# Kernel optimization log

Measured on AMD Instinct MI355X. Metric: run time of the kernel, lower is better.

## Reference

```python
import jax, jax.numpy as jnp
import numpy as np

NUM_BUCKETS = 320
MAX_DISTANCE = 800


def _layer_norm(x, w, b, eps=1e-5):
    x32 = x.astype(jnp.float32)
    mu = x32.mean(-1, keepdims=True)
    var = x32.var(-1, keepdims=True)
    return ((x32 - mu) / jnp.sqrt(var + eps) * w + b).astype(x.dtype)


def _rel_pos_bucket(rel):
    half = NUM_BUCKETS // 2            # 160
    st = half // 2                     # 80 (small threshold)
    sign = (rel >= 0).astype(jnp.int32)
    ab = jnp.abs(rel)
    is_small = ab < st
    log_ratio = jnp.log(jnp.clip(ab.astype(jnp.float32), 1.0) / st) / np.float32(np.log(MAX_DISTANCE / st))
    log_pos = st + (log_ratio * (half - st)).astype(jnp.int32)  # trunc toward zero like .long()
    log_pos = jnp.minimum(log_pos, half - 1)
    bucket = jnp.where(is_small, ab, log_pos) + sign * half
    return jnp.clip(bucket, 0, NUM_BUCKETS - 1)


def setup_inputs() -> dict:
    key = jax.random.key(0)
    B, T, C, H, FF = 2, 2048, 768, 12, 3072
    D = C // H
    ks = jax.random.split(key, 16)
    s = 0.02
    return {
        "x": jax.random.normal(ks[0], (B, T, C), jnp.float32),
        "ln1_w": jnp.ones((C,), jnp.float32),
        "ln1_b": jnp.zeros((C,), jnp.float32),
        "wq": jax.random.normal(ks[1], (C, C), jnp.float32) * s,
        "bq": jnp.zeros((C,), jnp.float32),
        "wk": jax.random.normal(ks[2], (C, C), jnp.float32) * s,
        "bk": jnp.zeros((C,), jnp.float32),
        "wv": jax.random.normal(ks[3], (C, C), jnp.float32) * s,
        "bv": jnp.zeros((C,), jnp.float32),
        "wo": jax.random.normal(ks[4], (C, C), jnp.float32) * s,
        "bo": jnp.zeros((C,), jnp.float32),
        "ln2_w": jnp.ones((C,), jnp.float32),
        "ln2_b": jnp.zeros((C,), jnp.float32),
        "w1": jax.random.normal(ks[5], (FF, C), jnp.float32) * s,
        "b1": jnp.zeros((FF,), jnp.float32),
        "w2": jax.random.normal(ks[6], (C, FF), jnp.float32) * s,
        "b2": jnp.zeros((C,), jnp.float32),
        "rel_embed": jax.random.normal(ks[7], (NUM_BUCKETS, H), jnp.float32),
        "gate_ur_w": jax.random.normal(ks[8], (H, D), jnp.float32) * 0.01,
        "gate_i_w": jax.random.normal(ks[9], (H, D), jnp.float32) * 0.01,
        "rel_scale": jnp.ones((H,), jnp.float32),
    }


def reference(x, ln1_w, ln1_b, wq, bq, wk, bk, wv, bv, wo, bo,
              ln2_w, ln2_b, w1, b1, w2, b2, rel_embed, gate_ur_w, gate_i_w, rel_scale):
    B, T, C = x.shape
    H = rel_embed.shape[1]
    D = C // H

    residual = x
    h = _layer_norm(x, ln1_w, ln1_b)
    q = (h @ wq.T + bq).reshape(B, T, H, D).transpose(0, 2, 1, 3)  # [B,H,T,D]
    k = (h @ wk.T + bk).reshape(B, T, H, D).transpose(0, 2, 1, 3)
    v = (h @ wv.T + bv).reshape(B, T, H, D).transpose(0, 2, 1, 3)

    attn = jnp.einsum('bhqd,bhkd->bhqk', q, k) * (D ** -0.5)

    # gated relative position bias
    pos = jnp.arange(T)
    rel = pos[None, :] - pos[:, None]                 # [T,T]
    buckets = _rel_pos_bucket(rel)                    # [T,T]
    pe = rel_embed[buckets]                           # [T,T,H]
    pe = jnp.transpose(pe, (2, 0, 1))[None]           # [1,H,T,T]
    g_in = q.mean(axis=2).transpose(0, 2, 1).mean(axis=-1)   # [B,D]
    gate_r = jax.nn.sigmoid(g_in @ gate_ur_w.T)       # [B,H]
    gate_u = jax.nn.sigmoid(g_in @ gate_i_w.T)        # [B,H]
    gate = 1.0 + (gate_u * rel_scale[None, :] * gate_r)[:, :, None, None]
    bias = pe * gate                                  # [B,H,T,T]

    attn = jax.nn.softmax(attn + bias, axis=-1)
    out = jnp.einsum('bhqk,bhkd->bhqd', attn, v).transpose(0, 2, 1, 3).reshape(B, T, C)
    x = residual + out @ wo.T + bo

    residual = x
    h = _layer_norm(x, ln2_w, ln2_b)
    h = jax.nn.gelu(h @ w1.T + b1, approximate=False) @ w2.T + b2
    return residual + h
```

## Files before the change

### kernel.cpp

```cpp
#include <hip/hip_runtime.h>
#include <hip/hip_bf16.h>


#define Tn 2048
#define Cn 768
#define Hn 12
#define Dn 64
#define FFn 3072
#define Mn 4096
#define QKVS 2304
#define LQK 1536

typedef __attribute__((ext_vector_type(8))) short bfrag;
typedef __attribute__((ext_vector_type(8))) unsigned short us8;
typedef __attribute__((ext_vector_type(4))) float f32x4;

#define GLDS(gptr, lptr) __builtin_amdgcn_global_load_lds( \
    (const __attribute__((address_space(1))) void*)(gptr), \
    (__attribute__((address_space(3))) void*)(lptr), 16, 0, 0)

#define SBAR()   __builtin_amdgcn_s_barrier()
#define WAITVM(N) asm volatile("s_waitcnt vmcnt(" #N ")" ::: "memory")
#define WAITLG0() asm volatile("s_waitcnt lgkmcnt(0)" ::: "memory")

#define QSCALE 0.18033688f
#define INVQS  5.5451774445f

__device__ __forceinline__ unsigned short f2bu(float f){
  __hip_bfloat16 h = __float2bfloat16(f);
  return *(unsigned short*)&h;
}
__device__ __forceinline__ float bu2f(unsigned short u){
  union { unsigned int i; float f; } v; v.i = ((unsigned int)u) << 16; return v.f;
}
__device__ __forceinline__ us8 pack8(float4 a, float4 b){
  us8 c;
  c[0]=f2bu(a.x); c[1]=f2bu(a.y); c[2]=f2bu(a.z); c[3]=f2bu(a.w);
  c[4]=f2bu(b.x); c[5]=f2bu(b.y); c[6]=f2bu(b.z); c[7]=f2bu(b.w);
  return c;
}
__device__ __forceinline__ float fexp2(float x){ return __builtin_amdgcn_exp2f(x); }

__device__ __forceinline__ float block_reduce_sum(float v, float* sred){
  #pragma unroll
  for (int off = 32; off > 0; off >>= 1) v += __shfl_down(v, off, 64);
  __syncthreads();
  if ((threadIdx.x & 63) == 0) sred[threadIdx.x >> 6] = v;
  __syncthreads();
  return sred[0] + sred[1] + sred[2] + sred[3];
}

__global__ __launch_bounds__(256) void cast_all_kernel(
    const float* __restrict__ wq, const float* __restrict__ wk,
    const float* __restrict__ wv, const float* __restrict__ wo,
    const float* __restrict__ w1, const float* __restrict__ w2,
    const float* __restrict__ bq, const float* __restrict__ bk,
    const float* __restrict__ bv, const float* __restrict__ rel_embed,
    unsigned short* __restrict__ Wqkv, unsigned short* __restrict__ Wob,
    unsigned short* __restrict__ W1b, unsigned short* __restrict__ W2b,
    float* __restrict__ bias_rel, float* __restrict__ bqkv)
{
  const int blk = blockIdx.x;
  if (blk >= 3472){
    const int i = (blk - 3472) * 256 + threadIdx.x;
    bqkv[i] = (i < Cn) ? bq[i] : (i < 2 * Cn) ? bk[i - Cn] : bv[i - 2 * Cn];
    return;
  }
  if (blk >= 3456){
    const int idx = (blk - 3456) * 256 + threadIdx.x;
    if (idx >= 4095) return;
    const int rel = idx - 2047;
    const int ab = rel < 0 ? -rel : rel;
    int bucket;
    if (ab < 80){
      bucket = ab;
    } else {
      const float lr = logf((float)ab * (1.0f / 80.0f)) * (1.0f / 2.3025851f);
      int lp = 80 + (int)(lr * 80.0f);
      bucket = lp < 159 ? lp : 159;
    }
    if (rel >= 0) bucket += 160;
    #pragma unroll
    for (int h = 0; h < Hn; h++)
      bias_rel[h * 4095 + idx] = rel_embed[bucket * Hn + h] * 1.44269504089f;
    return;
  }
  const float* src; unsigned short* dst; int i;
  if (blk < 288)      { src = wq; dst = Wqkv;               i = blk * 256 + threadIdx.x; }
  else if (blk < 576) { src = wk; dst = Wqkv + Cn * Cn;     i = (blk - 288) * 256 + threadIdx.x; }
  else if (blk < 864) { src = wv; dst = Wqkv + 2 * Cn * Cn; i = (blk - 576) * 256 + threadIdx.x; }
  else if (blk < 1152){ src = wo; dst = Wob;                i = (blk - 864) * 256 + threadIdx.x; }
  else if (blk < 2304){ src = w1; dst = W1b;                i = (blk - 1152) * 256 + threadIdx.x; }
  else                { src = w2; dst = W2b;                i = (blk - 2304) * 256 + threadIdx.x; }
  const float4 a = ((const float4*)src)[i * 2];
  const float4 b = ((const float4*)src)[i * 2 + 1];
  *(us8*)&dst[i * 8] = pack8(a, b);
}

__global__ __launch_bounds__(256) void ln_kernel(const float* __restrict__ xin,
    const float* __restrict__ w, const float* __restrict__ bsh,
    unsigned short* __restrict__ out)
{
  __shared__ float xs[Cn];
  __shared__ float sred[4];
  const size_t base = (size_t)blockIdx.x * Cn;
  float s = 0.f;
  for (int c = threadIdx.x; c < Cn; c += 256){
    float v = xin[base + c];
    xs[c] = v; s += v;
  }
  const float mean = block_reduce_sum(s, sred) * (1.f / Cn);
  float s2 = 0.f;
  for (int c = threadIdx.x; c < Cn; c += 256){
    float d = xs[c] - mean; s2 += d * d;
  }
  const float var = block_reduce_sum(s2, sred) * (1.f / Cn);
  const float rstd = rsqrtf(var + 1e-5f);
  for (int c = threadIdx.x; c < Cn; c += 256)
    out[base + c] = f2bu((xs[c] - mean) * rstd * w[c] + bsh[c]);
}

template<int EPI, bool TRANSV>
__global__ __launch_bounds__(256) void gemm_mfma_kernel(
    const unsigned short* __restrict__ A, const unsigned short* __restrict__ Bw,
    const float* __restrict__ bias, unsigned short* __restrict__ vt,
    void* __restrict__ Cout, int M, int N, int K, int ldo)
{
  __shared__ __align__(16) unsigned short As[2][128 * 32];
  __shared__ __align__(16) unsigned short Bs[2][64 * 32];
  const int tid = threadIdx.x;
  const int lane = tid & 63, w = tid >> 6;
  const int nl = lane & 15, quad = lane >> 4;
  const int wm = w >> 1, wn = w & 1;
  const int id = blockIdx.x;
  const int bm = ((id & 7) * 4 + ((id >> 3) & 3)) * 128;
  const int bn = (id >> 5) * 64;
  const int l4 = lane >> 2;
  const int lk = (((lane & 3) ^ ((lane >> 3) & 3)) * 8);
  const int qsw = (quad ^ ((nl >> 1) & 3)) * 8;

  f32x4 acc[4][2];
  #pragma unroll
  for (int i = 0; i < 4; i++)
    #pragma unroll
    for (int j = 0; j < 2; j++) acc[i][j] = (f32x4){0.f, 0.f, 0.f, 0.f};

  const unsigned short* A0 = A + (size_t)(bm + w * 16 + l4) * K + lk;
  const unsigned short* A1 = A + (size_t)(bm + (w + 4) * 16 + l4) * K + lk;
  const unsigned short* B0 = Bw + (size_t)(bn + w * 16 + l4) * K + lk;

  GLDS(A0, &As[0][w * 512]); GLDS(A1, &As[0][(w + 4) * 512]);
  GLDS(B0, &Bs[0][w * 512]);

  const int NIT = K >> 5;
  for (int t = 0; t < NIT; t++){
    const int cur = t & 1;
    SBAR();
    if (t + 1 < NIT){
      const int k0 = (t + 1) << 5;
      GLDS(A0 + k0, &As[cur ^ 1][w * 512]);
      GLDS(A1 + k0, &As[cur ^ 1][(w + 4) * 512]);
      GLDS(B0 + k0, &Bs[cur ^ 1][w * 512]);
      WAITVM(3);
    } else {
      WAITVM(0);
    }
    SBAR();
    bfrag Af[4], Bf[2];
    #pragma unroll
    for (int mt = 0; mt < 4; mt++)
      Af[mt] = *(const bfrag*)&As[cur][(wm * 64 + mt * 16 + nl) * 32 + qsw];
    #pragma unroll
    for (int nt = 0; nt < 2; nt++)
      Bf[nt] = *(const bfrag*)&Bs[cur][(wn * 32 + nt * 16 + nl) * 32 + qsw];
    #pragma unroll
    for (int mt = 0; mt < 4; mt++)
      #pragma unroll
      for (int nt = 0; nt < 2; nt++)
        acc[mt][nt] = __builtin_amdgcn_mfma_f32_16x16x32_bf16(Af[mt], Bf[nt], acc[mt][nt], 0, 0, 0);
  }

  if (TRANSV && bn >= 1536){
    #pragma unroll
    for (int nt = 0; nt < 2; nt++){
      const int col = bn + wn * 32 + nt * 16 + nl;
      const float bv_ = bias[col];
      const int vcol = col - 1536;
      #pragma unroll
      for (int mt = 0; mt < 4; mt++){
        const int row0 = bm + wm * 64 + mt * 16 + quad * 4;
        unsigned short pk[4];
        #pragma unroll
        for (int r = 0; r < 4; r++) pk[r] = f2bu(acc[mt][nt][r] + bv_);
        *(uint2*)&vt[(size_t)vcol * Mn + row0] = *(uint2*)pk;
      }
    }
    return;
  }
  #pragma unroll
  for (int nt = 0; nt < 2; nt++){
    const int col = bn + wn * 32 + nt * 16 + nl;
    const float bv_ = bias[col];
    const float sc = (EPI == 1 && col < Cn) ? QSCALE : 1.0f;
    #pragma unroll
    for (int mt = 0; mt < 4; mt++){
      const int row0 = bm + wm * 64 + mt * 16 + quad * 4;
      #pragma unroll
      for (int r = 0; r < 4; r++){
        const size_t idx = (size_t)(row0 + r) * ldo + col;
        const float v = acc[mt][nt][r] + bv_;
        if (EPI == 2){
          ((unsigned short*)Cout)[idx] = f2bu(0.5f * v * (1.f + erff(v * 0.70710678118f)));
        } else {
          ((unsigned short*)Cout)[idx] = f2bu(v * sc);
        }
      }
    }
  }
}

__global__ __launch_bounds__(256) void gemm_t64_kernel(
    const unsigned short* __restrict__ A, const unsigned short* __restrict__ Bw,
    const float* __restrict__ bias, const float* __restrict__ res,
    float* __restrict__ Cout, int M, int N, int K)
{
  __shared__ __align__(16) unsigned short As[2][2 * 64 * 32];
  __shared__ __align__(16) unsigned short Bs[2][2 * 64 * 32];
  const int tid = threadIdx.x;
  const int lane = tid & 63, w = tid >> 6;
  const int nl = lane & 15, quad = lane >> 4;
  const int id = blockIdx.x;
  const int bm = ((id & 7) * 8 + ((id >> 3) & 7)) * 64;
  const int bn = (id >> 6) * 64;
  const int l2 = lane >> 2;
  const int l3 = (((lane & 3) ^ ((lane >> 3) & 3)) * 8);
  const int qsw = (quad ^ ((nl >> 1) & 3)) * 8;

  f32x4 acc[4];
  #pragma unroll
  for (int j = 0; j < 4; j++) acc[j] = (f32x4){0.f, 0.f, 0.f, 0.f};

  const unsigned short* A0 = A + (size_t)(bm + w * 16 + l2) * K + l3;
  const unsigned short* B0 = Bw + (size_t)(bn + w * 16 + l2) * K + l3;

  GLDS(A0,      &As[0][w * 512]);
  GLDS(A0 + 32, &As[0][2048 + w * 512]);
  GLDS(B0,      &Bs[0][w * 512]);
  GLDS(B0 + 32, &Bs[0][2048 + w * 512]);

  const int NIT = K >> 6;
  for (int t = 0; t < NIT; t++){
    const int cur = t & 1;
    SBAR();
    if (t + 1 < NIT){
      const int k0 = (t + 1) << 6;
      GLDS(A0 + k0,      &As[cur ^ 1][w * 512]);
      GLDS(A0 + k0 + 32, &As[cur ^ 1][2048 + w * 512]);
      GLDS(B0 + k0,      &Bs[cur ^ 1][w * 512]);
      GLDS(B0 + k0 + 32, &Bs[cur ^ 1][2048 + w * 512]);
      WAITVM(4);
    } else {
      WAITVM(0);
    }
    SBAR();
    const bfrag Af0 = *(const bfrag*)&As[cur][(w * 16 + nl) * 32 + qsw];
    const bfrag Af1 = *(const bfrag*)&As[cur][2048 + (w * 16 + nl) * 32 + qsw];
    bfrag Bf0[4], Bf1[4];
    #pragma unroll
    for (int nt = 0; nt < 4; nt++){
      Bf0[nt] = *(const bfrag*)&Bs[cur][(nt * 16 + nl) * 32 + qsw];
      Bf1[nt] = *(const bfrag*)&Bs[cur][2048 + (nt * 16 + nl) * 32 + qsw];
    }
    #pragma unroll
    for (int nt = 0; nt < 4; nt++){
      acc[nt] = __builtin_amdgcn_mfma_f32_16x16x32_bf16(Af0, Bf0[nt], acc[nt], 0, 0, 0);
      acc[nt] = __builtin_amdgcn_mfma_f32_16x16x32_bf16(Af1, Bf1[nt], acc[nt], 0, 0, 0);
    }
  }

  const int row0 = bm + w * 16 + quad * 4;
  #pragma unroll
  for (int nt = 0; nt < 4; nt++){
    const int col = bn + nt * 16 + nl;
    const float bv_ = bias[col];
    #pragma unroll
    for (int r = 0; r < 4; r++){
      const size_t idx = (size_t)(row0 + r) * N + col;
      Cout[idx] = acc[nt][r] + bv_ + res[idx];
    }
  }
}

__global__ __launch_bounds__(256) void qmean_part_kernel(
    const unsigned short* __restrict__ QKVqk, float* __restrict__ qpart)
{
  __shared__ float ps[Cn];
  const int b = blockIdx.y, t0 = blockIdx.x * 128;
  const int tid = threadIdx.x;
  float a0 = 0.f, a1 = 0.f, a2 = 0.f;
  for (int r = 0; r < 128; r++){
    const size_t base = (size_t)(b * Tn + t0 + r) * LQK;
    a0 += bu2f(QKVqk[base + tid]);
    a1 += bu2f(QKVqk[base + tid + 256]);
    a2 += bu2f(QKVqk[base + tid + 512]);
  }
  ps[tid] = a0; ps[tid + 256] = a1; ps[tid + 512] = a2;
  __syncthreads();
  if (tid < Dn){
    float s = 0.f;
    #pragma unroll
    for (int hh = 0; hh < Hn; hh++) s += ps[hh * Dn + tid];
    qpart[(b * 16 + blockIdx.x) * Dn + tid] = s;
  }
}

__global__ __launch_bounds__(64) void gate_kernel(const float* __restrict__ qpart,
    const float* __restrict__ gur, const float* __restrict__ gi,
    const float* __restrict__ rsc, float* __restrict__ gate)
{
  const int b = blockIdx.x / Hn, h = blockIdx.x % Hn;
  const int d = threadIdx.x;
  float s = 0.f;
  #pragma unroll
  for (int blk = 0; blk < 16; blk++) s += qpart[(b * 16 + blk) * Dn + d];
  const float g = s * (1.f / (Hn * Tn)) * INVQS;
  float vr = g * gur[h * Dn + d];
  float vu = g * gi[h * Dn + d];
  #pragma unroll
  for (int off = 32; off > 0; off >>= 1){
    vr += __shfl_down(vr, off, 64);
    vu += __shfl_down(vu, off, 64);
  }
  if (d == 0){
    const float gr = 1.f / (1.f + __expf(-vr));
    const float gu = 1.f / (1.f + __expf(-vu));
    gate[blockIdx.x] = 1.f + gu * rsc[h] * gr;
  }
}

__global__ __launch_bounds__(256) void attn_mfma_kernel(
    const unsigned short* __restrict__ QKVqk, const unsigned short* __restrict__ VT,
    const float* __restrict__ bias_rel, const float* __restrict__ gate,
    unsigned short* __restrict__ O)
{
  __shared__ __align__(16) char smem[52224];
  unsigned short* Qs = (unsigned short*)smem;
  float* bias_blk    = (float*)smem;
  unsigned short* KsP = (unsigned short*)(smem + 9216);
  unsigned short* VtP = (unsigned short*)(smem + 25600);
  unsigned short* Ptq = (unsigned short*)(smem + 41984);
  float* lsh         = (float*)(smem + 51200);

  const int qbase = blockIdx.x * 64;
  const int h = blockIdx.y, b = blockIdx.z;
  const int tid = threadIdx.x;
  const float g = gate[b * Hn + h];
  const float* brow = bias_rel + h * 4095 + 1984 - qbase;
  const unsigned short* Q = QKVqk;
  const unsigned short* K = QKVqk + Cn;

  const int lane = tid & 63, w = tid >> 6;
  const int nl = lane & 15, quad = lane >> 4;
  const int l2 = lane >> 2;
  const int l3 = (((lane & 3) ^ ((lane >> 3) & 3)) * 8);
  const int qsw = (quad ^ ((nl >> 1) & 3)) * 8;

  const unsigned short* kg0 = K + (size_t)(b * Tn + w * 16 + l2) * LQK + h * Dn + l3;
  const unsigned short* vg0 = VT + (size_t)(h * Dn + w * 16 + l2) * Mn + (size_t)b * Tn + l3;

  GLDS(kg0,      KsP + w * 512);
  GLDS(kg0 + 32, KsP + 2048 + w * 512);
  GLDS(vg0,      VtP + w * 512);
  GLDS(vg0 + 32, VtP + 2048 + w * 512);

  {
    const int row = tid >> 2, cg = (tid & 3) * 16;
    const us8* qp = (const us8*)(Q + (size_t)(b * Tn + qbase + row) * LQK + h * Dn + cg);
    *(us8*)&Qs[row * 72 + cg]     = qp[0];
    *(us8*)&Qs[row * 72 + cg + 8] = qp[1];
  }
  __syncthreads();

  bfrag Qb[4][2];
  #pragma unroll
  for (int mt = 0; mt < 4; mt++){
    Qb[mt][0] = *(const bfrag*)&Qs[(mt * 16 + nl) * 72 + quad * 8];
    Qb[mt][1] = *(const bfrag*)&Qs[(mt * 16 + nl) * 72 + 32 + quad * 8];
  }
  __syncthreads();
  for (int j = tid; j < 2111; j += 256) bias_blk[j] = brow[j] * g;
  WAITLG0();

  const int wq = w & 1, wd = w >> 1;
  f32x4 Oa[2][2];
  #pragma unroll
  for (int a = 0; a < 2; a++)
    #pragma unroll
    for (int d0 = 0; d0 < 2; d0++) Oa[a][d0] = (f32x4){0.f, 0.f, 0.f, 0.f};
  float l_part[4] = {0.f, 0.f, 0.f, 0.f};

  for (int kt = 0; kt < 32; kt++){
    const int kbase = kt * 64;
    const int cur = (kt & 1) * 4096;
    const int nxt = 4096 - cur;
    SBAR();
    if (kt < 31){
      const unsigned short* kg = kg0 + (size_t)(kbase + 64) * LQK;
      const unsigned short* vg = vg0 + kbase + 64;
      GLDS(kg,      KsP + nxt + w * 512);
      GLDS(kg + 32, KsP + nxt + 2048 + w * 512);
      GLDS(vg,      VtP + nxt + w * 512);
      GLDS(vg + 32, VtP + nxt + 2048 + w * 512);
      WAITVM(4);
    } else {
      WAITVM(0);
    }

    const bfrag Ka0 = *(const bfrag*)&KsP[cur + (w * 16 + nl) * 32 + qsw];
    const bfrag Ka1 = *(const bfrag*)&KsP[cur + 2048 + (w * 16 + nl) * 32 + qsw];
    const int bofs = kbase + w * 16 + quad * 4 + 63 - nl;
    #pragma unroll
    for (int mt = 0; mt < 4; mt++){
      const float* bp = &bias_blk[bofs - mt * 16];
      f32x4 z = (f32x4){bp[0], bp[1], bp[2], bp[3]};
      z = __builtin_amdgcn_mfma_f32_16x16x32_bf16(Ka0, Qb[mt][0], z, 0, 0, 0);
      z = __builtin_amdgcn_mfma_f32_16x16x32_bf16(Ka1, Qb[mt][1], z, 0, 0, 0);
      const float p0 = fexp2(z[0]), p1 = fexp2(z[1]);
      const float p2 = fexp2(z[2]), p3 = fexp2(z[3]);
      l_part[mt] += (p0 + p1) + (p2 + p3);
      uint2 pk2;
      asm("v_cvt_pk_bf16_f32 %0, %1, %2" : "=v"(pk2.x) : "v"(p0), "v"(p1));
      asm("v_cvt_pk_bf16_f32 %0, %1, %2" : "=v"(pk2.y) : "v"(p2), "v"(p3));
      *(uint2*)&Ptq[(mt * 16 + nl) * 72 + w * 16 + quad * 4] = pk2;
    }
    WAITLG0();
    SBAR();

    bfrag Vf[2][2], Pf[2][2];
    #pragma unroll
    for (int d0 = 0; d0 < 2; d0++){
      const int dt = wd * 2 + d0;
      Vf[d0][0] = *(const bfrag*)&VtP[cur + (dt * 16 + nl) * 32 + qsw];
      Vf[d0][1] = *(const bfrag*)&VtP[cur + 2048 + (dt * 16 + nl) * 32 + qsw];
    }
    #pragma unroll
    for (int a = 0; a < 2; a++){
      const int qt = wq * 2 + a;
      Pf[a][0] = *(const bfrag*)&Ptq[(qt * 16 + nl) * 72 + quad * 8];
      Pf[a][1] = *(const bfrag*)&Ptq[(qt * 16 + nl) * 72 + 32 + quad * 8];
    }
    #pragma unroll
    for (int a = 0; a < 2; a++)
      #pragma unroll
      for (int d0 = 0; d0 < 2; d0++){
        Oa[a][d0] = __builtin_amdgcn_mfma_f32_16x16x32_bf16(Vf[d0][0], Pf[a][0], Oa[a][d0], 0, 0, 0);
        Oa[a][d0] = __builtin_amdgcn_mfma_f32_16x16x32_bf16(Vf[d0][1], Pf[a][1], Oa[a][d0], 0, 0, 0);
      }
  }

  #pragma unroll
  for (int mt = 0; mt < 4; mt++){
    float l = l_part[mt];
    l += __shfl_xor(l, 16, 64);
    l += __shfl_xor(l, 32, 64);
    if (quad == 0) lsh[w * 64 + mt * 16 + nl] = l;
  }
  __syncthreads();
  #pragma unroll
  for (int a = 0; a < 2; a++){
    const int q = (wq * 2 + a) * 16 + nl;
    const float linv = 1.f / (lsh[q] + lsh[64 + q] + lsh[128 + q] + lsh[192 + q]);
    unsigned short* orow = O + (size_t)(b * Tn + qbase + q) * Cn + h * Dn;
    #pragma unroll
    for (int d0 = 0; d0 < 2; d0++){
      unsigned short pk[4];
      #pragma unroll
      for (int r = 0; r < 4; r++) pk[r] = f2bu(Oa[a][d0][r] * linv);
      *(uint2*)&orow[(wd * 2 + d0) * 16 + quad * 4] = *(uint2*)pk;
    }
  }
}

extern "C" void kernel_launch(void* const* d_in, const int* in_sizes, int n_in,
                              void* d_out, int out_size, void* d_ws, size_t ws_size,
                              hipStream_t stream)
{
  const float* x     = (const float*)d_in[0];
  const float* ln1_w = (const float*)d_in[1];
  const float* ln1_b = (const float*)d_in[2];
  const float* wq    = (const float*)d_in[3];
  const float* bq    = (const float*)d_in[4];
  const float* wk    = (const float*)d_in[5];
  const float* bk    = (const float*)d_in[6];
  const float* wv    = (const float*)d_in[7];
  const float* bv    = (const float*)d_in[8];
  const float* wo    = (const float*)d_in[9];
  const float* bo    = (const float*)d_in[10];
  const float* ln2_w = (const float*)d_in[11];
  const float* ln2_b = (const float*)d_in[12];
  const float* w1    = (const float*)d_in[13];
  const float* b1    = (const float*)d_in[14];
  const float* w2    = (const float*)d_in[15];
  const float* b2    = (const float*)d_in[16];
  const float* rel_embed = (const float*)d_in[17];
  const float* gur   = (const float*)d_in[18];
  const float* gi    = (const float*)d_in[19];
  const float* rsc   = (const float*)d_in[20];

  char* ws = (char*)d_ws;
  unsigned short* QKVqk = (unsigned short*)(ws);
  unsigned short* VT    = (unsigned short*)(ws + 12582912);
  unsigned short* Ob    = (unsigned short*)(ws + 18874368);
  float*          X2    = (float*)(ws + 25165824);
  unsigned short* Hb    = (unsigned short*)(ws + 37748736);
  unsigned short* Wqkv  = (unsigned short*)(ws + 44040192);
  unsigned short* Wob   = (unsigned short*)(ws + 47579136);
  unsigned short* W1b   = (unsigned short*)(ws + 48758784);
  unsigned short* W2b   = (unsigned short*)(ws + 53477376);
  float*          bqkv  = (float*)(ws + 58195968);
  float*          bias_rel = (float*)(ws + 58205184);
  float*          qpart = (float*)(ws + 58401744);
  float*          gate  = (float*)(ws + 58409936);
  unsigned short* Fb    = (unsigned short*)(ws);

  cast_all_kernel<<<3481, 256, 0, stream>>>(wq, wk, wv, wo, w1, w2, bq, bk, bv,
                                            rel_embed, Wqkv, Wob, W1b, W2b,
                                            bias_rel, bqkv);
  ln_kernel<<<Mn, 256, 0, stream>>>(x, ln1_w, ln1_b, Hb);
  gemm_mfma_kernel<1, true><<<(QKVS / 64) * (Mn / 128), 256, 0, stream>>>(
      Hb, Wqkv, bqkv, VT, QKVqk, Mn, QKVS, Cn, LQK);
  qmean_part_kernel<<<dim3(16, 2), 256, 0, stream>>>(QKVqk, qpart);
  gate_kernel<<<2 * Hn, 64, 0, stream>>>(qpart, gur, gi, rsc, gate);
  attn_mfma_kernel<<<dim3(Tn / 64, Hn, 2), 256, 0, stream>>>(QKVqk, VT, bias_rel, gate, Ob);
  gemm_t64_kernel<<<(Cn / 64) * (Mn / 64), 256, 0, stream>>>(
      Ob, Wob, bo, x, X2, Mn, Cn, Cn);
  ln_kernel<<<Mn, 256, 0, stream>>>(X2, ln2_w, ln2_b, Hb);
  gemm_mfma_kernel<2, false><<<(FFn / 64) * (Mn / 128), 256, 0, stream>>>(
      Hb, W1b, b1, nullptr, Fb, Mn, FFn, Cn, FFn);
  gemm_t64_kernel<<<(Cn / 64) * (Mn / 64), 256, 0, stream>>>(
      Fb, W2b, b2, X2, (float*)d_out, Mn, Cn, FFn);
}
```

Baseline: 323.1 us.

## Split attention into producer and consumer wavefronts with double-buffered P tile

The attention kernel moves to 512 threads. Four producer waves compute QK^T plus bias, exp, and write P into a double-buffered LDS tile. Four consumer waves load V tiles and run the P·V MFMAs one iteration behind, so the softmax and PV stages overlap instead of being serialized by a mid-loop barrier. This raises LDS use and threads per block, which may lower occupancy, and consumer waves get higher scheduling priority during their MFMAs.

```diff
diff --git a/kernel.cpp b/kernel.cpp
--- a/kernel.cpp
+++ b/kernel.cpp
@@ -338,18 +338,18 @@
   }
 }
 
-__global__ __launch_bounds__(256) void attn_mfma_kernel(
+__global__ __launch_bounds__(512) void attn_mfma_kernel(
     const unsigned short* __restrict__ QKVqk, const unsigned short* __restrict__ VT,
     const float* __restrict__ bias_rel, const float* __restrict__ gate,
     unsigned short* __restrict__ O)
 {
-  __shared__ __align__(16) char smem[52224];
+  __shared__ __align__(16) char smem[61440];
   unsigned short* Qs = (unsigned short*)smem;
   float* bias_blk    = (float*)smem;
   unsigned short* KsP = (unsigned short*)(smem + 9216);
   unsigned short* VtP = (unsigned short*)(smem + 25600);
   unsigned short* Ptq = (unsigned short*)(smem + 41984);
-  float* lsh         = (float*)(smem + 51200);
+  float* lsh         = (float*)(smem + 60416);
 
   const int qbase = blockIdx.x * 64;
   const int h = blockIdx.y, b = blockIdx.z;
@@ -365,118 +365,137 @@
   const int l3 = (((lane & 3) ^ ((lane >> 3) & 3)) * 8);
   const int qsw = (quad ^ ((nl >> 1) & 3)) * 8;
 
-  const unsigned short* kg0 = K + (size_t)(b * Tn + w * 16 + l2) * LQK + h * Dn + l3;
-  const unsigned short* vg0 = VT + (size_t)(h * Dn + w * 16 + l2) * Mn + (size_t)b * Tn + l3;
-
-  GLDS(kg0,      KsP + w * 512);
-  GLDS(kg0 + 32, KsP + 2048 + w * 512);
-  GLDS(vg0,      VtP + w * 512);
-  GLDS(vg0 + 32, VtP + 2048 + w * 512);
+  const bool prod = (w < 4);
+  const int sw = prod ? w : (w - 4);
+
+  const unsigned short* kg0 = K + (size_t)(b * Tn + sw * 16 + l2) * LQK + h * Dn + l3;
+  const unsigned short* vg0 = VT + (size_t)(h * Dn + sw * 16 + l2) * Mn + (size_t)b * Tn + l3;
+
+  if (prod){
+    GLDS(kg0,      KsP + sw * 512);
+    GLDS(kg0 + 32, KsP + 2048 + sw * 512);
+  }
 
   {
-    const int row = tid >> 2, cg = (tid & 3) * 16;
+    const int row = tid >> 3, cg = (tid & 7) * 8;
     const us8* qp = (const us8*)(Q + (size_t)(b * Tn + qbase + row) * LQK + h * Dn + cg);
-    *(us8*)&Qs[row * 72 + cg]     = qp[0];
-    *(us8*)&Qs[row * 72 + cg + 8] = qp[1];
+    *(us8*)&Qs[row * 72 + cg] = qp[0];
   }
   __syncthreads();
 
   bfrag Qb[4][2];
-  #pragma unroll
-  for (int mt = 0; mt < 4; mt++){
-    Qb[mt][0] = *(const bfrag*)&Qs[(mt * 16 + nl) * 72 + quad * 8];
-    Qb[mt][1] = *(const bfrag*)&Qs[(mt * 16 + nl) * 72 + 32 + quad * 8];
+  if (prod){
+    #pragma unroll
+    for (int mt = 0; mt < 4; mt++){
+      Qb[mt][0] = *(const bfrag*)&Qs[(mt * 16 + nl) * 72 + quad * 8];
+      Qb[mt][1] = *(const bfrag*)&Qs[(mt * 16 + nl) * 72 + 32 + quad * 8];
+    }
   }
   __syncthreads();
-  for (int j = tid; j < 2111; j += 256) bias_blk[j] = brow[j] * g;
+  for (int j = tid; j < 2111; j += 512) bias_blk[j] = brow[j] * g;
   WAITLG0();
 
-  const int wq = w & 1, wd = w >> 1;
-  f32x4 Oa[2][2];
-  #pragma unroll
-  for (int a = 0; a < 2; a++)
-    #pragma unroll
-    for (int d0 = 0; d0 < 2; d0++) Oa[a][d0] = (f32x4){0.f, 0.f, 0.f, 0.f};
+  f32x4 Oa[4];
+  #pragma unroll
+  for (int a = 0; a < 4; a++) Oa[a] = (f32x4){0.f, 0.f, 0.f, 0.f};
   float l_part[4] = {0.f, 0.f, 0.f, 0.f};
 
   for (int kt = 0; kt < 32; kt++){
     const int kbase = kt * 64;
-    const int cur = (kt & 1) * 4096;
-    const int nxt = 4096 - cur;
+    const int curP = (kt & 1) * 4608;
     SBAR();
-    if (kt < 31){
-      const unsigned short* kg = kg0 + (size_t)(kbase + 64) * LQK;
-      const unsigned short* vg = vg0 + kbase + 64;
-      GLDS(kg,      KsP + nxt + w * 512);
-      GLDS(kg + 32, KsP + nxt + 2048 + w * 512);
-      GLDS(vg,      VtP + nxt + w * 512);
-      GLDS(vg + 32, VtP + nxt + 2048 + w * 512);
-      WAITVM(4);
+    if (prod){
+      const int curK = (kt & 1) * 4096;
+      if (kt < 31){
+        const unsigned short* kg = kg0 + (size_t)(kbase + 64) * LQK;
+        GLDS(kg,      KsP + (4096 - curK) + sw * 512);
+        GLDS(kg + 32, KsP + (4096 - curK) + 2048 + sw * 512);
+        WAITVM(2);
+      } else {
+        WAITVM(0);
+      }
+      const bfrag Ka0 = *(const bfrag*)&KsP[curK + (sw * 16 + nl) * 32 + qsw];
+      const bfrag Ka1 = *(const bfrag*)&KsP[curK + 2048 + (sw * 16 + nl) * 32 + qsw];
+      const int bofs = kbase + sw * 16 + quad * 4 + 63 - nl;
+      #pragma unroll
+      for (int mt = 0; mt < 4; mt++){
+        const float* bp = &bias_blk[bofs - mt * 16];
+        f32x4 z = (f32x4){bp[0], bp[1], bp[2], bp[3]};
+        z = __builtin_amdgcn_mfma_f32_16x16x32_bf16(Ka0, Qb[mt][0], z, 0, 0, 0);
+        z = __builtin_amdgcn_mfma_f32_16x16x32_bf16(Ka1, Qb[mt][1], z, 0, 0, 0);
+        const float p0 = fexp2(z[0]), p1 = fexp2(z[1]);
+        const float p2 = fexp2(z[2]), p3 = fexp2(z[3]);
+        l_part[mt] += (p0 + p1) + (p2 + p3);
+        uint2 pk2;
+        asm("v_cvt_pk_bf16_f32 %0, %1, %2" : "=v"(pk2.x) : "v"(p0), "v"(p1));
+        asm("v_cvt_pk_bf16_f32 %0, %1, %2" : "=v"(pk2.y) : "v"(p2), "v"(p3));
+        *(uint2*)&Ptq[curP + (mt * 16 + nl) * 72 + sw * 16 + quad * 4] = pk2;
+      }
+      WAITLG0();
     } else {
-      WAITVM(0);
-    }
-
-    const bfrag Ka0 = *(const bfrag*)&KsP[cur + (w * 16 + nl) * 32 + qsw];
-    const bfrag Ka1 = *(const bfrag*)&KsP[cur + 2048 + (w * 16 + nl) * 32 + qsw];
-    const int bofs = kbase + w * 16 + quad * 4 + 63 - nl;
+      const int vbuf = (kt & 1) * 4096;
+      const unsigned short* vg = vg0 + kbase;
+      GLDS(vg,      VtP + vbuf + sw * 512);
+      GLDS(vg + 32, VtP + vbuf + 2048 + sw * 512);
+      WAITVM(2);
+      if (kt > 0){
+        const int vprev = 4096 - vbuf;
+        const int prvP = 4608 - curP;
+        const bfrag Vf0 = *(const bfrag*)&VtP[vprev + (sw * 16 + nl) * 32 + qsw];
+        const bfrag Vf1 = *(const bfrag*)&VtP[vprev + 2048 + (sw * 16 + nl) * 32 + qsw];
+        bfrag Pf[4][2];
+        #pragma unroll
+        for (int a = 0; a < 4; a++){
+          Pf[a][0] = *(const bfrag*)&Ptq[prvP + (a * 16 + nl) * 72 + quad * 8];
+          Pf[a][1] = *(const bfrag*)&Ptq[prvP + (a * 16 + nl) * 72 + 32 + quad * 8];
+        }
+        __builtin_amdgcn_s_setprio(1);
+        #pragma unroll
+        for (int a = 0; a < 4; a++){
+          Oa[a] = __builtin_amdgcn_mfma_f32_16x16x32_bf16(Vf0, Pf[a][0], Oa[a], 0, 0, 0);
+          Oa[a] = __builtin_amdgcn_mfma_f32_16x16x32_bf16(Vf1, Pf[a][1], Oa[a], 0, 0, 0);
+        }
+        __builtin_amdgcn_s_setprio(0);
+      }
+    }
+  }
+
+  SBAR();
+  if (prod){
     #pragma unroll
     for (int mt = 0; mt < 4; mt++){
-      const float* bp = &bias_blk[bofs - mt * 16];
-      f32x4 z = (f32x4){bp[0], bp[1], bp[2], bp[3]};
-      z = __builtin_amdgcn_mfma_f32_16x16x32_bf16(Ka0, Qb[mt][0], z, 0, 0, 0);
-      z = __builtin_amdgcn_mfma_f32_16x16x32_bf16(Ka1, Qb[mt][1], z, 0, 0, 0);
-      const float p0 = fexp2(z[0]), p1 = fexp2(z[1]);
-      const float p2 = fexp2(z[2]), p3 = fexp2(z[3]);
-      l_part[mt] += (p0 + p1) + (p2 + p3);
-      uint2 pk2;
-      asm("v_cvt_pk_bf16_f32 %0, %1, %2" : "=v"(pk2.x) : "v"(p0), "v"(p1));
-      asm("v_cvt_pk_bf16_f32 %0, %1, %2" : "=v"(pk2.y) : "v"(p2), "v"(p3));
-      *(uint2*)&Ptq[(mt * 16 + nl) * 72 + w * 16 + quad * 4] = pk2;
-    }
-    WAITLG0();
-    SBAR();
-
-    bfrag Vf[2][2], Pf[2][2];
-    #pragma unroll
-    for (int d0 = 0; d0 < 2; d0++){
-      const int dt = wd * 2 + d0;
-      Vf[d0][0] = *(const bfrag*)&VtP[cur + (dt * 16 + nl) * 32 + qsw];
-      Vf[d0][1] = *(const bfrag*)&VtP[cur + 2048 + (dt * 16 + nl) * 32 + qsw];
-    }
-    #pragma unroll
-    for (int a = 0; a < 2; a++){
-      const int qt = wq * 2 + a;
-      Pf[a][0] = *(const bfrag*)&Ptq[(qt * 16 + nl) * 72 + quad * 8];
-      Pf[a][1] = *(const bfrag*)&Ptq[(qt * 16 + nl) * 72 + 32 + quad * 8];
-    }
-    #pragma unroll
-    for (int a = 0; a < 2; a++)
-      #pragma unroll
-      for (int d0 = 0; d0 < 2; d0++){
-        Oa[a][d0] = __builtin_amdgcn_mfma_f32_16x16x32_bf16(Vf[d0][0], Pf[a][0], Oa[a][d0], 0, 0, 0);
-        Oa[a][d0] = __builtin_amdgcn_mfma_f32_16x16x32_bf16(Vf[d0][1], Pf[a][1], Oa[a][d0], 0, 0, 0);
-      }
-  }
-
-  #pragma unroll
-  for (int mt = 0; mt < 4; mt++){
-    float l = l_part[mt];
-    l += __shfl_xor(l, 16, 64);
-    l += __shfl_xor(l, 32, 64);
-    if (quad == 0) lsh[w * 64 + mt * 16 + nl] = l;
+      float l = l_part[mt];
+      l += __shfl_xor(l, 16, 64);
+      l += __shfl_xor(l, 32, 64);
+      if (quad == 0) lsh[sw * 64 + mt * 16 + nl] = l;
+    }
+  } else {
+    WAITVM(0);
+    const bfrag Vf0 = *(const bfrag*)&VtP[4096 + (sw * 16 + nl) * 32 + qsw];
+    const bfrag Vf1 = *(const bfrag*)&VtP[4096 + 2048 + (sw * 16 + nl) * 32 + qsw];
+    bfrag Pf[4][2];
+    #pragma unroll
+    for (int a = 0; a < 4; a++){
+      Pf[a][0] = *(const bfrag*)&Ptq[4608 + (a * 16 + nl) * 72 + quad * 8];
+      Pf[a][1] = *(const bfrag*)&Ptq[4608 + (a * 16 + nl) * 72 + 32 + quad * 8];
+    }
+    #pragma unroll
+    for (int a = 0; a < 4; a++){
+      Oa[a] = __builtin_amdgcn_mfma_f32_16x16x32_bf16(Vf0, Pf[a][0], Oa[a], 0, 0, 0);
+      Oa[a] = __builtin_amdgcn_mfma_f32_16x16x32_bf16(Vf1, Pf[a][1], Oa[a], 0, 0, 0);
+    }
   }
   __syncthreads();
-  #pragma unroll
-  for (int a = 0; a < 2; a++){
-    const int q = (wq * 2 + a) * 16 + nl;
-    const float linv = 1.f / (lsh[q] + lsh[64 + q] + lsh[128 + q] + lsh[192 + q]);
-    unsigned short* orow = O + (size_t)(b * Tn + qbase + q) * Cn + h * Dn;
-    #pragma unroll
-    for (int d0 = 0; d0 < 2; d0++){
+  if (!prod){
+    #pragma unroll
+    for (int a = 0; a < 4; a++){
+      const int q = a * 16 + nl;
+      const float linv = 1.f / (lsh[q] + lsh[64 + q] + lsh[128 + q] + lsh[192 + q]);
+      unsigned short* orow = O + (size_t)(b * Tn + qbase + q) * Cn + h * Dn;
       unsigned short pk[4];
       #pragma unroll
-      for (int r = 0; r < 4; r++) pk[r] = f2bu(Oa[a][d0][r] * linv);
-      *(uint2*)&orow[(wd * 2 + d0) * 16 + quad * 4] = *(uint2*)pk;
+      for (int r = 0; r < 4; r++) pk[r] = f2bu(Oa[a][r] * linv);
+      *(uint2*)&orow[sw * 16 + quad * 4] = *(uint2*)pk;
     }
   }
 }
@@ -531,7 +550,7 @@
       Hb, Wqkv, bqkv, VT, QKVqk, Mn, QKVS, Cn, LQK);
   qmean_part_kernel<<<dim3(16, 2), 256, 0, stream>>>(QKVqk, qpart);
   gate_kernel<<<2 * Hn, 64, 0, stream>>>(qpart, gur, gi, rsc, gate);
-  attn_mfma_kernel<<<dim3(Tn / 64, Hn, 2), 256, 0, stream>>>(QKVqk, VT, bias_rel, gate, Ob);
+  attn_mfma_kernel<<<dim3(Tn / 64, Hn, 2), 512, 0, stream>>>(QKVqk, VT, bias_rel, gate, Ob);
   gemm_t64_kernel<<<(Cn / 64) * (Mn / 64), 256, 0, stream>>>(
       Ob, Wob, bo, x, X2, Mn, Cn, Cn);
   ln_kernel<<<Mn, 256, 0, stream>>>(X2, ln2_w, ln2_b, Hb);
```

After: 336.8 us. 1.04x slower.
